# Optimization experiments

Hardware: AMD Instinct MI355X
Metric: run time of the kernel (lower is better)

## Reference

```python
import jax, jax.numpy as jnp
import numpy as np

M, B, T, C, H, HS = 2, 8, 1024, 512, 8, 64
EPS = 1e-5

NAMES = ['x','sa_kw1','sa_kb1','sa_kw2','sa_qw1','sa_qb1','sa_qw2','sa_vw1','sa_vb1','sa_vw2',
         'sa_pw1','sa_pb1','sa_pw2','sa_pb2','ff_w1','ff_b1','ff_w2','ff_b2',
         'ln1_g','ln1_b','ln2_g','ln2_b','lnc_g','lnc_b',
         'ca_qw','ca_kvw','ca_pw1','ca_pb1','ca_pw2','ca_pb2']


def setup_inputs() -> dict:
    key = jax.random.key(0)
    it = iter(jax.random.split(key, 40))
    def w(shape, s=0.02):
        return jax.random.normal(next(it), shape, jnp.float32) * s
    d = {}
    d['x'] = jax.random.normal(next(it), (M, B, T, C), jnp.float32)
    # self-attention heads: Linear(C,HS//2)+bias -> tanh -> Linear(HS//2,HS) no bias, stacked over (M,H)
    for nm in ('k', 'q', 'v'):
        d['sa_%sw1' % nm] = w((M, H, C, HS // 2))
        d['sa_%sb1' % nm] = jnp.zeros((M, H, HS // 2), jnp.float32)
        d['sa_%sw2' % nm] = w((M, H, HS // 2, HS))
    # MHA output proj: Linear(H*HS,C//2)->tanh->Linear(C//2,C)
    d['sa_pw1'] = w((M, H * HS, C // 2)); d['sa_pb1'] = jnp.zeros((M, C // 2), jnp.float32)
    d['sa_pw2'] = w((M, C // 2, C));      d['sa_pb2'] = jnp.zeros((M, C), jnp.float32)
    # feed-forward
    d['ff_w1'] = w((M, C, 4 * C)); d['ff_b1'] = jnp.zeros((M, 4 * C), jnp.float32)
    d['ff_w2'] = w((M, 4 * C, C)); d['ff_b2'] = jnp.zeros((M, C), jnp.float32)
    # layernorms
    for nm in ('ln1', 'ln2', 'lnc'):
        d[nm + '_g'] = jnp.ones((M, C), jnp.float32)
        d[nm + '_b'] = jnp.zeros((M, C), jnp.float32)
    # cross-attention: per head q proj (no bias), per-kv-modality kv proj (no bias, 2*HS)
    d['ca_qw'] = w((M, H, C, HS))
    d['ca_kvw'] = w((M, H, M - 1, C, 2 * HS))
    d['ca_pw1'] = w((M, H * HS, C // 2)); d['ca_pb1'] = jnp.zeros((M, C // 2), jnp.float32)
    d['ca_pw2'] = w((M, C // 2, C));      d['ca_pb2'] = jnp.zeros((M, C), jnp.float32)
    return d


def _ln(x, g, b):
    mu = x.mean(-1, keepdims=True)
    var = ((x - mu) ** 2).mean(-1, keepdims=True)
    return (x - mu) * jax.lax.rsqrt(var + EPS) * g + b


def _attend(q, k, v, mask):
    # q,k,v: (B,H,T,HS); causal masked softmax attention
    aff = jnp.einsum('bhtd,bhsd->bhts', q, k) * (HS ** -0.5)
    aff = jnp.where(mask, aff, -jnp.inf)
    return jnp.einsum('bhts,bhsd->bhtd', jax.nn.softmax(aff, axis=-1), v)


def _merge(o):
    # (B,H,T,HS) -> (B,T,H*HS), matching torch.cat over heads
    return o.transpose(0, 2, 1, 3).reshape(o.shape[0], o.shape[2], -1)


def _forward(p):
    mask = jnp.tril(jnp.ones((T, T), bool))
    x = p['x']
    attended = []
    for i in range(M):  # fixed small modality loop
        xi = x[i]
        h = _ln(xi, p['ln1_g'][i], p['ln1_b'][i])
        def hm(w1, b1, w2):
            # batched over heads: Linear->tanh->Linear
            z = jnp.tanh(jnp.einsum('btc,hce->bhte', h, w1) + b1[:, None, :])
            return jnp.einsum('bhte,hed->bhtd', z, w2)
        o = _attend(hm(p['sa_qw1'][i], p['sa_qb1'][i], p['sa_qw2'][i]),
                    hm(p['sa_kw1'][i], p['sa_kb1'][i], p['sa_kw2'][i]),
                    hm(p['sa_vw1'][i], p['sa_vb1'][i], p['sa_vw2'][i]), mask)
        o = jnp.tanh(_merge(o) @ p['sa_pw1'][i] + p['sa_pb1'][i]) @ p['sa_pw2'][i] + p['sa_pb2'][i]
        xi = xi + o
        h2 = _ln(xi, p['ln2_g'][i], p['ln2_b'][i])
        xi = xi + (jax.nn.relu(h2 @ p['ff_w1'][i] + p['ff_b1'][i]) @ p['ff_w2'][i] + p['ff_b2'][i])
        attended.append(xi)
    outs = []
    for i in range(M):
        xi = attended[i]
        hq = _ln(xi, p['lnc_g'][i], p['lnc_b'][i])
        q = jnp.einsum('btc,hcd->bhtd', hq, p['ca_qw'][i])
        acc = 0.0
        for jidx, j in enumerate([j for j in range(M) if j != i]):
            kv = jnp.einsum('btc,hcd->bhtd', attended[j], p['ca_kvw'][i][:, jidx])
            k, v = jnp.split(kv, 2, axis=-1)
            acc = acc + _attend(q, k, v, mask)
        o = jnp.tanh(_merge(acc) @ p['ca_pw1'][i] + p['ca_pb1'][i]) @ p['ca_pw2'][i] + p['ca_pb2'][i]
        outs.append(xi + o)
    return jnp.stack(outs)


def reference(x, sa_kw1, sa_kb1, sa_kw2, sa_qw1, sa_qb1, sa_qw2, sa_vw1, sa_vb1, sa_vw2,
              sa_pw1, sa_pb1, sa_pw2, sa_pb2, ff_w1, ff_b1, ff_w2, ff_b2,
              ln1_g, ln1_b, ln2_g, ln2_b, lnc_g, lnc_b,
              ca_qw, ca_kvw, ca_pw1, ca_pb1, ca_pw2, ca_pb2):
    args = (x, sa_kw1, sa_kb1, sa_kw2, sa_qw1, sa_qb1, sa_qw2, sa_vw1, sa_vb1, sa_vw2,
            sa_pw1, sa_pb1, sa_pw2, sa_pb2, ff_w1, ff_b1, ff_w2, ff_b2,
            ln1_g, ln1_b, ln2_g, ln2_b, lnc_g, lnc_b,
            ca_qw, ca_kvw, ca_pw1, ca_pb1, ca_pw2, ca_pb2)
    return _forward(dict(zip(NAMES, args)))
```

## Files before the change

### kernel.cpp

```cpp
#include <hip/hip_runtime.h>
#include <hip/hip_bf16.h>

#define DEVI __device__ __forceinline__

typedef __attribute__((ext_vector_type(8))) short short8v;
typedef __attribute__((ext_vector_type(4))) short short4v;
typedef __attribute__((ext_vector_type(4))) float float4v;
typedef __attribute__((ext_vector_type(16))) float f32x16;

#if defined(__has_builtin)
#if __has_builtin(__builtin_amdgcn_exp2f)
#define EXP2F(x) __builtin_amdgcn_exp2f(x)
#endif
#endif
#ifndef EXP2F
#define EXP2F(x) exp2f(x)
#endif

constexpr int Mm = 2, Bb = 8, Tt = 1024, Cc = 512, Hh = 8, HSs = 64;
constexpr int ROWS = Bb * Tt;
constexpr size_t BTC = (size_t)Bb * Tt * Cc;
constexpr size_t SLAB = (size_t)ROWS * 512;
constexpr size_t KOFF = (size_t)2 * ROWS * 768;
constexpr size_t VOFF = KOFF + 2 * SLAB;
constexpr float SCQ = 0.18033688011112042f;

DEVI short f2bf(float f) {
    __hip_bfloat16 h = __float2bfloat16(f);
    short s; __builtin_memcpy(&s, &h, 2); return s;
}

DEVI float4v mfma16(short8v a, short8v b, float4v c) {
    return __builtin_amdgcn_mfma_f32_16x16x32_bf16(a, b, c, 0, 0, 0);
}
DEVI f32x16 mfma32(short8v a, short8v b, f32x16 c) {
    return __builtin_amdgcn_mfma_f32_32x32x16_bf16(a, b, c, 0, 0, 0);
}

DEVI void gload_lds16(const short* g, short* l) {
    __builtin_amdgcn_global_load_lds(
        (const __attribute__((address_space(1))) void*)g,
        (__attribute__((address_space(3))) void*)l, 16, 0, 0);
}

struct TDesc {
    const float* src; short* dst;
    int K, N;
    long long moff, hoff;
    int base;
};
struct TPack { TDesc d[14]; };

__global__ __launch_bounds__(256) void transpose_all(TPack p) {
    __shared__ float t[32][33];
    int bid = blockIdx.x;
    int di = 0;
#pragma unroll
    for (int i = 1; i < 14; i++) if (bid >= p.d[i].base) di = i;
    TDesc d = p.d[di];
    int local = bid - d.base;
    int kb = d.K >> 5, nb = d.N >> 5;
    int bx = local % kb; int rest = local / kb;
    int by = rest % nb;  int z = rest / nb;
    int k0 = bx * 32, n0 = by * 32;
    size_t so = (size_t)z * d.K * d.N;
    short* dst = d.dst + (size_t)(z >> 3) * d.moff + (size_t)(z & 7) * d.hoff;
    int tx = threadIdx.x & 31, ty = threadIdx.x >> 5;
#pragma unroll
    for (int i = 0; i < 32; i += 8)
        t[ty + i][tx] = d.src[so + (size_t)(k0 + ty + i) * d.N + n0 + tx];
    __syncthreads();
#pragma unroll
    for (int i = 0; i < 32; i += 8)
        dst[(size_t)(n0 + ty + i) * d.K + k0 + tx] = f2bf(t[tx][ty + i]);
}

__global__ __launch_bounds__(256) void bias_cat3(const float* __restrict__ q,
                                                 const float* __restrict__ k,
                                                 const float* __restrict__ v,
                                                 float* __restrict__ o) {
    int m = blockIdx.x, t = threadIdx.x;
    o[m * 768 + t]       = q[m * 256 + t];
    o[m * 768 + 256 + t] = k[m * 256 + t];
    o[m * 768 + 512 + t] = v[m * 256 + t];
}

__global__ __launch_bounds__(256) void vtrans(const short* __restrict__ V,
                                              short* __restrict__ VT,
                                              int vrs, int hs, long long vzs) {
    __shared__ short t[32][33];
    int t0 = blockIdx.x * 32, d0 = blockIdx.y * 32;
    int z = blockIdx.z, mod = z >> 6, bh = z & 63, b = bh >> 3, h = bh & 7;
    const short* src = V + (long long)mod * vzs + (size_t)b * Tt * vrs + h * hs;
    short* dst = VT + (size_t)z * 65536;
    int tx = threadIdx.x, ty = threadIdx.y;
#pragma unroll
    for (int i = 0; i < 32; i += 8)
        t[ty + i][tx] = src[(size_t)(t0 + ty + i) * vrs + d0 + tx];
    __syncthreads();
#pragma unroll
    for (int i = 0; i < 32; i += 8)
        dst[(size_t)(d0 + ty + i) * Tt + t0 + tx] = t[tx][ty + i];
}

__global__ __launch_bounds__(256) void ln_kernel(const float* __restrict__ x,
                                                 const float* __restrict__ g,
                                                 const float* __restrict__ b,
                                                 short* __restrict__ out, size_t xzs) {
    int z = blockIdx.y;
    x += z * xzs; g += z * Cc; b += z * Cc; out += z * SLAB;
    int row = blockIdx.x * 4 + (threadIdx.x >> 6);
    int l = threadIdx.x & 63;
    const float* xr = x + (size_t)row * Cc;
    float4 a = *(const float4*)&xr[l * 4];
    float4 c = *(const float4*)&xr[256 + l * 4];
    float s = (a.x + a.y) + (a.z + a.w) + (c.x + c.y) + (c.z + c.w);
    float q = (a.x * a.x + a.y * a.y) + (a.z * a.z + a.w * a.w) +
              (c.x * c.x + c.y * c.y) + (c.z * c.z + c.w * c.w);
#pragma unroll
    for (int o = 1; o < 64; o <<= 1) { s += __shfl_xor(s, o, 64); q += __shfl_xor(q, o, 64); }
    float mu = s * (1.f / Cc);
    float var = q * (1.f / Cc) - mu * mu;
    float rs = rsqrtf(var + 1e-5f);
    float4 ga = *(const float4*)&g[l * 4],   gc = *(const float4*)&g[256 + l * 4];
    float4 ba = *(const float4*)&b[l * 4],   bc = *(const float4*)&b[256 + l * 4];
    short4v o1, o2;
    o1[0] = f2bf((a.x - mu) * rs * ga.x + ba.x);
    o1[1] = f2bf((a.y - mu) * rs * ga.y + ba.y);
    o1[2] = f2bf((a.z - mu) * rs * ga.z + ba.z);
    o1[3] = f2bf((a.w - mu) * rs * ga.w + ba.w);
    o2[0] = f2bf((c.x - mu) * rs * gc.x + bc.x);
    o2[1] = f2bf((c.y - mu) * rs * gc.y + bc.y);
    o2[2] = f2bf((c.z - mu) * rs * gc.z + bc.z);
    o2[3] = f2bf((c.w - mu) * rs * gc.w + bc.w);
    short* orow = out + (size_t)row * Cc;
    *(short4v*)&orow[l * 4]       = o1;
    *(short4v*)&orow[256 + l * 4] = o2;
}

template<int BM, int BN, int ACT, bool BIAS, bool RES, bool WF, bool WB>
__global__ __launch_bounds__(256, 2) void gemm2(
    const short* __restrict__ A, int lda, long long a_zs,
    const short* __restrict__ Wt, int ldw, long long w_zs,
    const float* __restrict__ bias, long long bias_zs,
    const float* __restrict__ res, long long res_zs,
    float* __restrict__ outF, long long outF_zs,
    short* __restrict__ outB, long long outB_zs,
    int ldc, int K, float oscale) {
    constexpr int BK = 64;
    __shared__ short As[BM][BK];
    __shared__ short Bs[BN][BK];
    long long z = blockIdx.z;
    A += z * a_zs; Wt += z * w_zs;
    if (BIAS) bias += z * bias_zs;
    if (RES)  res  += z * res_zs;
    if (WF)   outF += z * outF_zs;
    if (WB)   outB += z * outB_zs;
    int m0 = blockIdx.x * BM, n0 = blockIdx.y * BN;
    int tid = threadIdx.x, wv = tid >> 6, l = tid & 63, lr = l & 15, lg = l >> 4;
    constexpr int WM = BM / 2, WN = BN / 2;
    int wm = wv & 1, wn = wv >> 1;
    constexpr int AI = WM / 16, BJ = WN / 16;
    float4v acc[AI][BJ] = {};
    int lrow = l >> 3;
    int gcol = (l & 7) ^ lrow;
    constexpr int CHA = BM / 8, CHB = BN / 8;
    for (int k0 = 0; k0 < K; k0 += BK) {
        __syncthreads();
#pragma unroll
        for (int c = 0; c < CHA / 4; c++) {
            int ch = wv + c * 4;
            gload_lds16(&A[(size_t)(m0 + ch * 8 + lrow) * lda + k0 + gcol * 8],
                        &As[ch * 8][0]);
        }
#pragma unroll
        for (int c = 0; c < CHB / 4; c++) {
            int ch = wv + c * 4;
            gload_lds16(&Wt[(size_t)(n0 + ch * 8 + lrow) * ldw + k0 + gcol * 8],
                        &Bs[ch * 8][0]);
        }
        __syncthreads();
#pragma unroll
        for (int kk = 0; kk < 2; kk++) {
            int g = (kk * 4 + lg) ^ (lr & 7);
            short8v af[AI], bfv[BJ];
#pragma unroll
            for (int i = 0; i < AI; i++)
                af[i] = *(const short8v*)&As[wm * WM + i * 16 + lr][g * 8];
#pragma unroll
            for (int j = 0; j < BJ; j++)
                bfv[j] = *(const short8v*)&Bs[wn * WN + j * 16 + lr][g * 8];
#pragma unroll
            for (int i = 0; i < AI; i++)
#pragma unroll
                for (int j = 0; j < BJ; j++)
                    acc[i][j] = mfma16(af[i], bfv[j], acc[i][j]);
        }
    }
#pragma unroll
    for (int i = 0; i < AI; i++) {
#pragma unroll
        for (int j = 0; j < BJ; j++) {
            int col = n0 + wn * WN + j * 16 + lr;
            float bv = BIAS ? bias[col] : 0.f;
#pragma unroll
            for (int r = 0; r < 4; r++) {
                int row = m0 + wm * WM + i * 16 + lg * 4 + r;
                float v = acc[i][j][r] * oscale + bv;
                if (ACT == 1) v = tanhf(v);
                if (ACT == 2) v = fmaxf(v, 0.f);
                size_t idx = (size_t)row * ldc + col;
                if (RES) v += res[idx];
                if (WF) outF[idx] = v;
                if (WB) outB[idx] = f2bf(v);
            }
        }
    }
}

template<int ACT, bool BIAS, bool RES, bool WF, bool WB>
__global__ __launch_bounds__(256, 2) void gemm3(
    const short* __restrict__ A, int lda, long long a_zs,
    const short* __restrict__ Wt, int ldw, long long w_zs,
    const float* __restrict__ bias, long long bias_zs,
    const float* __restrict__ res, long long res_zs,
    float* __restrict__ outF, long long outF_zs,
    short* __restrict__ outB, long long outB_zs,
    int ldc, int K, float oscale) {
    constexpr int BM = 128, BN = 128, BK = 64;
    __shared__ short As[2][BM][BK];
    __shared__ short Bs[2][BN][BK];
    long long z = blockIdx.z;
    A += z * a_zs; Wt += z * w_zs;
    if (BIAS) bias += z * bias_zs;
    if (RES)  res  += z * res_zs;
    if (WF)   outF += z * outF_zs;
    if (WB)   outB += z * outB_zs;
    int m0 = blockIdx.x * BM, n0 = blockIdx.y * BN;
    int tid = threadIdx.x, wv = tid >> 6, l = tid & 63;
    int lq = l & 31, hi = l >> 5;
    int wm = wv & 1, wn = wv >> 1;
    f32x16 acc[2][2] = {};
    int lrow = l >> 3;
    int gcol = (l & 7) ^ lrow;

    auto STAGE = [&](int bi, int k0) {
#pragma unroll
        for (int c = 0; c < 4; c++) {
            int ch = wv + c * 4;
            gload_lds16(&A[(size_t)(m0 + ch * 8 + lrow) * lda + k0 + gcol * 8],
                        &As[bi][ch * 8][0]);
        }
#pragma unroll
        for (int c = 0; c < 4; c++) {
            int ch = wv + c * 4;
            gload_lds16(&Wt[(size_t)(n0 + ch * 8 + lrow) * ldw + k0 + gcol * 8],
                        &Bs[bi][ch * 8][0]);
        }
    };

    STAGE(0, 0);
    __syncthreads();
    int NT = K / BK;
    for (int t = 0; t < NT; t++) {
        int cur = t & 1;
        if (t + 1 < NT) STAGE(cur ^ 1, (t + 1) * BK);
        const short (*Ac)[BK] = As[cur];
        const short (*Bc)[BK] = Bs[cur];
#pragma unroll
        for (int ks = 0; ks < 4; ks++) {
            int g = (ks * 2 + hi) ^ (lq & 7);
            short8v af[2], bf[2];
#pragma unroll
            for (int i = 0; i < 2; i++)
                af[i] = *(const short8v*)&Ac[wm * 64 + i * 32 + lq][g * 8];
#pragma unroll
            for (int j = 0; j < 2; j++)
                bf[j] = *(const short8v*)&Bc[wn * 64 + j * 32 + lq][g * 8];
#pragma unroll
            for (int i = 0; i < 2; i++)
#pragma unroll
                for (int j = 0; j < 2; j++)
                    acc[i][j] = mfma32(af[i], bf[j], acc[i][j]);
        }
        __syncthreads();
    }
#pragma unroll
    for (int i = 0; i < 2; i++) {
#pragma unroll
        for (int j = 0; j < 2; j++) {
            int col = n0 + wn * 64 + j * 32 + lq;
            float bv = BIAS ? bias[col] : 0.f;
#pragma unroll
            for (int r = 0; r < 16; r++) {
                int row = m0 + wm * 64 + i * 32 + 4 * hi + (r & 3) + 8 * (r >> 2);
                float v = acc[i][j][r] * oscale + bv;
                if (ACT == 1) v = tanhf(v);
                if (ACT == 2) v = fmaxf(v, 0.f);
                size_t idx = (size_t)row * ldc + col;
                if (RES) v += res[idx];
                if (WF) outF[idx] = v;
                if (WB) outB[idx] = f2bf(v);
            }
        }
    }
}

__global__ __launch_bounds__(256) void proj2(const short* __restrict__ Z,
                                             const short* __restrict__ W2,
                                             short* __restrict__ Qo,
                                             short* __restrict__ Ko,
                                             short* __restrict__ VTo,
                                             float qscale) {
    __shared__ short As[64][40], Ws[64][40];
    __shared__ short Tv[64][72];
    int zz = blockIdx.y, t = zz >> 4, m = (zz >> 3) & 1, h = zz & 7;
    int m0 = blockIdx.x * 64;
    const short* Ap = Z + (size_t)m * ((size_t)ROWS * 768) + t * 256 + h * 32;
    const short* Wp = W2 + (size_t)zz * 2048;
    float sc = (t == 0) ? qscale : 1.0f;
    int tid = threadIdx.x, w = tid >> 6, l = tid & 63, lr = l & 15, lg = l >> 4;
    int r = tid >> 2, c = (tid & 3) * 8;
    *(short8v*)&As[r][c] = *(const short8v*)&Ap[(size_t)(m0 + r) * 768 + c];
    *(short8v*)&Ws[r][c] = *(const short8v*)&Wp[r * 32 + c];
    __syncthreads();
    short8v af = *(const short8v*)&As[w * 16 + lr][lg * 8];
    float4v acc[4] = {};
#pragma unroll
    for (int j = 0; j < 4; j++) {
        short8v bf = *(const short8v*)&Ws[j * 16 + lr][lg * 8];
        acc[j] = mfma16(af, bf, acc[j]);
    }
    if (t < 2) {
        short* Op = (t == 0 ? Qo : Ko) + (size_t)m * SLAB + h * 64;
#pragma unroll
        for (int j = 0; j < 4; j++)
#pragma unroll
            for (int rr = 0; rr < 4; rr++)
                Op[(size_t)(m0 + w * 16 + lg * 4 + rr) * 512 + j * 16 + lr] =
                    f2bf(acc[j][rr] * sc);
    } else {
#pragma unroll
        for (int j = 0; j < 4; j++)
#pragma unroll
            for (int rr = 0; rr < 4; rr++)
                Tv[j * 16 + lr][w * 16 + lg * 4 + rr] = f2bf(acc[j][rr]);
        __syncthreads();
        int b = m0 >> 10, trow0 = m0 & 1023;
        int z64 = m * 64 + b * 8 + h;
        short* dst = VTo + (size_t)z64 * 65536;
        int d = w * 16 + (l >> 2), toff = (l & 3) * 16;
        *(short8v*)&dst[(size_t)d * Tt + trow0 + toff]     = *(const short8v*)&Tv[d][toff];
        *(short8v*)&dst[(size_t)d * Tt + trow0 + toff + 8] = *(const short8v*)&Tv[d][toff + 8];
    }
}

__global__ __launch_bounds__(512, 4) void flash_attn4(
    const short* __restrict__ Q, const short* __restrict__ K,
    const short* __restrict__ VT, short* __restrict__ O,
    int krs, int khs, long long qzs, long long kzs, long long vtzs, long long ozs)
{
    __shared__ short Ks[2][64][64];
    __shared__ short Vs[2][64][64];
    int id = blockIdx.x;
    int bh = id & 63, mod = (id >> 6) & 1, p = (id >> 7) & 3;
    Q += (long long)mod * qzs; K += (long long)mod * kzs;
    VT += (long long)mod * vtzs; O += (long long)mod * ozs;
    int b = bh >> 3, h = bh & 7;
    int tid = threadIdx.x, w = tid >> 6, l = tid & 63;
    int lq = l & 31, hi = l >> 5;
    int strip = (w < 4) ? p : 7 - p;
    int qwb = strip * 128 + (w & 3) * 32;
    int qabs = qwb + lq;
    const short* Qp = Q + (size_t)b * Tt * Cc + h * HSs;
    const short* Kp = K + (size_t)b * Tt * krs + h * khs;
    const short* Vp = VT + (size_t)bh * HSs * Tt;
    short* Op = O + (size_t)b * Tt * Cc + h * HSs;

    short8v qf[4];
#pragma unroll
    for (int c = 0; c < 4; c++)
        qf[c] = *(const short8v*)&Qp[(size_t)qabs * Cc + (c * 2 + hi) * 8];

    f32x16 oacc[2] = {};
    float mrun = -1e30f, lrun = 0.f;
    int nk = 2 * (7 - p) + 2;
    short8v pk, pv;

    auto LOADT = [&](int kb) {
        int r = tid >> 3, cg = (tid & 7) ^ (r & 7);
        pk = *(const short8v*)&Kp[(size_t)(kb + r) * krs + cg * 8];
        pv = *(const short8v*)&Vp[(size_t)r * Tt + kb + cg * 8];
    };
    auto STORET = [&](int bi) {
        int r = tid >> 3, cp = tid & 7;
        *(short8v*)&Ks[bi][r][cp * 8] = pk;
        *(short8v*)&Vs[bi][r][cp * 8] = pv;
    };

    LOADT(0); STORET(0); __syncthreads();

    for (int t = 0; t < nk; t++) {
        int cur = t & 1, kb = t * 64;
        bool pre = (t + 1 < nk);
        if (pre) LOADT(kb + 64);
        if (kb <= qwb + 31) {
            bool full = (kb + 63 <= qwb);
            f32x16 st[2] = {};
            __builtin_amdgcn_s_setprio(1);
#pragma unroll
            for (int kh = 0; kh < 2; kh++) {
#pragma unroll
                for (int cc = 0; cc < 4; cc++) {
                    int r = kh * 32 + lq;
                    int cp = (cc * 2 + hi) ^ (r & 7);
                    short8v af = *(const short8v*)&Ks[cur][r][cp * 8];
                    st[kh] = mfma32(af, qf[cc], st[kh]);
                }
            }
            __builtin_amdgcn_s_setprio(0);
            float pr[32];
            if (full) {
#pragma unroll
                for (int kh = 0; kh < 2; kh++)
#pragma unroll
                    for (int r = 0; r < 16; r++) pr[kh * 16 + r] = st[kh][r];
            } else {
#pragma unroll
                for (int kh = 0; kh < 2; kh++)
#pragma unroll
                    for (int r = 0; r < 16; r++) {
                        int kabs = kb + kh * 32 + (r & 3) + 8 * (r >> 2) + 4 * hi;
                        pr[kh * 16 + r] = (kabs <= qabs) ? st[kh][r] : -3.0e38f;
                    }
            }
            float t16[16];
#pragma unroll
            for (int i = 0; i < 16; i++) t16[i] = fmaxf(pr[i], pr[i + 16]);
#pragma unroll
            for (int i = 0; i < 8; i++) t16[i] = fmaxf(t16[i], t16[i + 8]);
            float mx = fmaxf(fmaxf(fmaxf(t16[0], t16[4]), fmaxf(t16[1], t16[5])),
                             fmaxf(fmaxf(t16[2], t16[6]), fmaxf(t16[3], t16[7])));
            mx = fmaxf(mx, __shfl_xor(mx, 32));
            if (!__all(mx <= mrun + 11.5f)) {
                float mn = fmaxf(mrun, mx);
                float al = EXP2F(mrun - mn);
                mrun = mn;
                lrun *= al;
#pragma unroll
                for (int dh = 0; dh < 2; dh++)
#pragma unroll
                    for (int r = 0; r < 16; r++) oacc[dh][r] *= al;
            }
#pragma unroll
            for (int i = 0; i < 32; i++) pr[i] = EXP2F(pr[i] - mrun);
            float s16[16];
#pragma unroll
            for (int i = 0; i < 16; i++) s16[i] = pr[i] + pr[i + 16];
#pragma unroll
            for (int i = 0; i < 8; i++) s16[i] = s16[i] + s16[i + 8];
            float rsum = ((s16[0] + s16[4]) + (s16[1] + s16[5])) +
                         ((s16[2] + s16[6]) + (s16[3] + s16[7]));
            rsum += __shfl_xor(rsum, 32);
            lrun += rsum;
#pragma unroll
            for (int ks = 0; ks < 4; ks++) {
                unsigned x0, x1, y0, y1;
                asm("v_cvt_pk_bf16_f32 %0, %1, %2" : "=v"(x0) : "v"(pr[ks*8+0]), "v"(pr[ks*8+1]));
                asm("v_cvt_pk_bf16_f32 %0, %1, %2" : "=v"(x1) : "v"(pr[ks*8+2]), "v"(pr[ks*8+3]));
                asm("v_cvt_pk_bf16_f32 %0, %1, %2" : "=v"(y0) : "v"(pr[ks*8+4]), "v"(pr[ks*8+5]));
                asm("v_cvt_pk_bf16_f32 %0, %1, %2" : "=v"(y1) : "v"(pr[ks*8+6]), "v"(pr[ks*8+7]));
                asm volatile("v_permlane32_swap_b32 %0, %1" : "+v"(x0), "+v"(y0));
                asm volatile("v_permlane32_swap_b32 %0, %1" : "+v"(x1), "+v"(y1));
                union { unsigned u[4]; short8v s; } uu;
                uu.u[0] = x0; uu.u[1] = x1; uu.u[2] = y0; uu.u[3] = y1;
                __builtin_amdgcn_s_setprio(1);
#pragma unroll
                for (int dh = 0; dh < 2; dh++) {
                    int r = dh * 32 + lq;
                    int cp = (ks * 2 + hi) ^ (r & 7);
                    short8v vf = *(const short8v*)&Vs[cur][r][cp * 8];
                    oacc[dh] = mfma32(vf, uu.s, oacc[dh]);
                }
                __builtin_amdgcn_s_setprio(0);
            }
        }
        if (pre) STORET(cur ^ 1);
        __syncthreads();
    }
    float inv = 1.f / lrun;
#pragma unroll
    for (int dh = 0; dh < 2; dh++)
#pragma unroll
        for (int r = 0; r < 16; r += 2) {
            unsigned wds;
            float a0 = oacc[dh][r] * inv, a1 = oacc[dh][r + 1] * inv;
            asm("v_cvt_pk_bf16_f32 %0, %1, %2" : "=v"(wds) : "v"(a0), "v"(a1));
            int d = (r & 3) + 8 * (r >> 2) + 4 * hi + dh * 32;
            *(unsigned*)&Op[(size_t)qabs * Cc + d] = wds;
        }
}

extern "C" void kernel_launch(void* const* d_in, const int* in_sizes, int n_in,
                              void* d_out, int out_size, void* d_ws, size_t ws_size,
                              hipStream_t stream) {
    (void)in_sizes; (void)n_in; (void)out_size; (void)ws_size;
    const float* X     = (const float*)d_in[0];
    const float* saKW1 = (const float*)d_in[1];
    const float* saKB1 = (const float*)d_in[2];
    const float* saKW2 = (const float*)d_in[3];
    const float* saQW1 = (const float*)d_in[4];
    const float* saQB1 = (const float*)d_in[5];
    const float* saQW2 = (const float*)d_in[6];
    const float* saVW1 = (const float*)d_in[7];
    const float* saVB1 = (const float*)d_in[8];
    const float* saVW2 = (const float*)d_in[9];
    const float* saPW1 = (const float*)d_in[10];
    const float* saPB1 = (const float*)d_in[11];
    const float* saPW2 = (const float*)d_in[12];
    const float* saPB2 = (const float*)d_in[13];
    const float* ffW1  = (const float*)d_in[14];
    const float* ffB1  = (const float*)d_in[15];
    const float* ffW2  = (const float*)d_in[16];
    const float* ffB2  = (const float*)d_in[17];
    const float* ln1g  = (const float*)d_in[18];
    const float* ln1b  = (const float*)d_in[19];
    const float* ln2g  = (const float*)d_in[20];
    const float* ln2b  = (const float*)d_in[21];
    const float* lncg  = (const float*)d_in[22];
    const float* lncb  = (const float*)d_in[23];
    const float* caQW  = (const float*)d_in[24];
    const float* caKVW = (const float*)d_in[25];
    const float* caPW1 = (const float*)d_in[26];
    const float* caPB1 = (const float*)d_in[27];
    const float* caPW2 = (const float*)d_in[28];
    const float* caPB2 = (const float*)d_in[29];
    float* OUT = (float*)d_out;

    char* ws = (char*)d_ws;
    size_t cur = 0;
    auto alloc = [&](size_t bytes) -> char* {
        char* p = ws + cur; cur += (bytes + 255) & ~(size_t)255; return p;
    };

    short* WT = (short*)alloc((size_t)7700480 * 2);
    size_t wo = 0;
    auto wslot = [&](size_t e) -> short* { short* p = WT + wo; wo += e; return p; };
    short* w_qkv1 = wslot(786432);
    short* w_qkv2 = wslot(98304);
    short* w_pw1 = wslot(262144); short* w_pw2 = wslot(262144);
    short* w_ff1 = wslot(2097152); short* w_ff2 = wslot(2097152);
    short* w_caq = wslot(524288);  short* w_cakv = wslot(1048576);
    short* w_cp1 = wslot(262144);  short* w_cp2 = wslot(262144);
    float* bqkv = (float*)alloc(2 * 768 * 4);

    short* Hb  = (short*)alloc(2 * SLAB * 2);
    short* Qb  = (short*)alloc(2 * SLAB * 2);
    short* Obf = (short*)alloc(2 * SLAB * 2);
    short* Fb  = (short*)alloc((size_t)2 * ROWS * 2048 * 2);
    short* AB  = (short*)alloc(2 * SLAB * 2);
    short* VTb = Hb;
    short* P1b = Hb;
    short* Kb = Fb + KOFF;

    TPack tp;
    int base = 0, ti = 0;
    auto addT = [&](const float* s, short* d, int K, int N, int slices,
                    long long moff, long long hoff) {
        tp.d[ti++] = TDesc{s, d, K, N, moff, hoff, base};
        base += (K / 32) * (N / 32) * slices;
    };
    addT(saQW1, w_qkv1,          512, 32, 16, 393216, 16384);
    addT(saKW1, w_qkv1 + 131072, 512, 32, 16, 393216, 16384);
    addT(saVW1, w_qkv1 + 262144, 512, 32, 16, 393216, 16384);
    addT(saQW2, w_qkv2,          32, 64, 16, 16384, 2048);
    addT(saKW2, w_qkv2 + 32768,  32, 64, 16, 16384, 2048);
    addT(saVW2, w_qkv2 + 65536,  32, 64, 16, 16384, 2048);
    addT(saPW1, w_pw1, 512, 256, 2, 0, 131072);
    addT(saPW2, w_pw2, 256, 512, 2, 0, 131072);
    addT(ffW1,  w_ff1, 512, 2048, 2, 0, 1048576);
    addT(ffW2,  w_ff2, 2048, 512, 2, 0, 1048576);
    addT(caQW,  w_caq, 512, 64, 16, 262144, 32768);
    addT(caKVW, w_cakv, 512, 128, 16, 524288, 65536);
    addT(caPW1, w_cp1, 512, 256, 2, 0, 131072);
    addT(caPW2, w_cp2, 256, 512, 2, 0, 131072);
    transpose_all<<<dim3(base), 256, 0, stream>>>(tp);
    bias_cat3<<<2, 256, 0, stream>>>(saQB1, saKB1, saVB1, bqkv);

    dim3 tb32(32, 8, 1);

    ln_kernel<<<dim3(ROWS / 4, 2), 256, 0, stream>>>(X, ln1g, ln1b, Hb, BTC);
    gemm2<128, 128, 1, true, false, false, true><<<dim3(64, 6, 2), 256, 0, stream>>>(
        Hb, 512, SLAB, w_qkv1, 512, 393216, bqkv, 768,
        nullptr, 0, nullptr, 0, Fb, (long long)ROWS * 768, 768, 512, 1.0f);
    proj2<<<dim3(128, 48), 256, 0, stream>>>(Fb, w_qkv2, Qb, Kb, VTb, SCQ);
    flash_attn4<<<dim3(512), 512, 0, stream>>>(
        Qb, Kb, VTb, Obf, 512, 64, SLAB, SLAB, 4194304, SLAB);
    gemm2<64, 128, 1, true, false, false, true><<<dim3(128, 2, 2), 256, 0, stream>>>(
        Obf, 512, SLAB, w_pw1, 512, 131072, saPB1, 256,
        nullptr, 0, nullptr, 0, P1b, (long long)ROWS * 256, 256, 512, 1.0f);
    gemm2<64, 128, 0, true, true, true, false><<<dim3(128, 4, 2), 256, 0, stream>>>(
        P1b, 256, (long long)ROWS * 256, w_pw2, 256, 131072, saPB2, 512,
        X, BTC, OUT, BTC, nullptr, 0, 512, 256, 1.0f);
    ln_kernel<<<dim3(ROWS / 4, 2), 256, 0, stream>>>(OUT, ln2g, ln2b, Hb, BTC);
    gemm2<128, 128, 2, true, false, false, true><<<dim3(64, 16, 2), 256, 0, stream>>>(
        Hb, 512, SLAB, w_ff1, 512, 1048576, ffB1, 2048,
        nullptr, 0, nullptr, 0, Fb, (long long)ROWS * 2048, 2048, 512, 1.0f);
    gemm3<0, true, true, true, true><<<dim3(64, 4, 2), 256, 0, stream>>>(
        Fb, 2048, (long long)ROWS * 2048, w_ff2, 2048, 1048576, ffB2, 512,
        OUT, BTC, OUT, BTC, AB, SLAB, 512, 2048, 1.0f);

    ln_kernel<<<dim3(ROWS / 4, 2), 256, 0, stream>>>(OUT, lncg, lncb, Hb, BTC);
    gemm2<64, 128, 0, false, false, false, true><<<dim3(128, 4, 2), 256, 0, stream>>>(
        Hb, 512, SLAB, w_caq, 512, 262144, nullptr, 0,
        nullptr, 0, nullptr, 0, Qb, SLAB, 512, 512, SCQ);
    gemm2<128, 128, 0, false, false, false, true><<<dim3(64, 8, 2), 256, 0, stream>>>(
        AB + SLAB, 512, -(long long)SLAB, w_cakv, 512, 524288, nullptr, 0,
        nullptr, 0, nullptr, 0, Fb, (long long)ROWS * 1024, 1024, 512, 1.0f);
    vtrans<<<dim3(32, 2, 128), tb32, 0, stream>>>(Fb + 64, VTb, 1024, 128, (long long)ROWS * 1024);
    flash_attn4<<<dim3(512), 512, 0, stream>>>(
        Qb, Fb, VTb, Obf, 1024, 128, SLAB, (long long)ROWS * 1024, 4194304, SLAB);
    gemm2<64, 128, 1, true, false, false, true><<<dim3(128, 2, 2), 256, 0, stream>>>(
        Obf, 512, SLAB, w_cp1, 512, 131072, caPB1, 256,
        nullptr, 0, nullptr, 0, P1b, (long long)ROWS * 256, 256, 512, 1.0f);
    gemm2<64, 128, 0, true, true, true, false><<<dim3(128, 4, 2), 256, 0, stream>>>(
        P1b, 256, (long long)ROWS * 256, w_cp2, 256, 131072, caPB2, 512,
        OUT, BTC, OUT, BTC, nullptr, 0, 512, 256, 1.0f);
}
```

Baseline: 355.3 us.

## Fuse output-projection MLP pairs and fold V transpose into KV GEMM epilogue

Replaces each pair of output-projection GEMMs (Linear→tanh→Linear plus residual) with one kernel that keeps the 32x256 tanh intermediate in shared memory, avoiding a global round trip of the intermediate and one launch per projection. The cross-attention KV GEMM now writes K directly and transposes the V half through LDS in its epilogue, removing the separate vtrans kernel. The fused projection kernel reads A and weights straight from global memory without LDS staging, so the GEMM part may run at lower efficiency than the tiled gemm2 it replaces.

```diff
diff --git a/kernel.cpp b/kernel.cpp
--- a/kernel.cpp
+++ b/kernel.cpp
@@ -22,7 +22,6 @@
 constexpr size_t BTC = (size_t)Bb * Tt * Cc;
 constexpr size_t SLAB = (size_t)ROWS * 512;
 constexpr size_t KOFF = (size_t)2 * ROWS * 768;
-constexpr size_t VOFF = KOFF + 2 * SLAB;
 constexpr float SCQ = 0.18033688011112042f;
 
 DEVI short f2bf(float f) {
@@ -83,24 +82,6 @@
     o[m * 768 + t]       = q[m * 256 + t];
     o[m * 768 + 256 + t] = k[m * 256 + t];
     o[m * 768 + 512 + t] = v[m * 256 + t];
-}
-
-__global__ __launch_bounds__(256) void vtrans(const short* __restrict__ V,
-                                              short* __restrict__ VT,
-                                              int vrs, int hs, long long vzs) {
-    __shared__ short t[32][33];
-    int t0 = blockIdx.x * 32, d0 = blockIdx.y * 32;
-    int z = blockIdx.z, mod = z >> 6, bh = z & 63, b = bh >> 3, h = bh & 7;
-    const short* src = V + (long long)mod * vzs + (size_t)b * Tt * vrs + h * hs;
-    short* dst = VT + (size_t)z * 65536;
-    int tx = threadIdx.x, ty = threadIdx.y;
-#pragma unroll
-    for (int i = 0; i < 32; i += 8)
-        t[ty + i][tx] = src[(size_t)(t0 + ty + i) * vrs + d0 + tx];
-    __syncthreads();
-#pragma unroll
-    for (int i = 0; i < 32; i += 8)
-        dst[(size_t)(d0 + ty + i) * Tt + t0 + tx] = t[tx][ty + i];
 }
 
 __global__ __launch_bounds__(256) void ln_kernel(const float* __restrict__ x,
@@ -218,6 +199,88 @@
     }
 }
 
+__global__ __launch_bounds__(256, 2) void gemm_kv(
+    const short* __restrict__ A, long long a_zs,
+    const short* __restrict__ Wt, long long w_zs,
+    short* __restrict__ outB, long long outB_zs,
+    short* __restrict__ VTo, int K) {
+    constexpr int BK = 64;
+    __shared__ short As[128][BK];
+    __shared__ short Bs[128][BK];
+    __shared__ short Tv[64][136];
+    long long z = blockIdx.z;
+    A += z * a_zs; Wt += z * w_zs; outB += z * outB_zs;
+    int m0 = blockIdx.x * 128, n0 = blockIdx.y * 128;
+    int tid = threadIdx.x, wv = tid >> 6, l = tid & 63, lr = l & 15, lg = l >> 4;
+    int wm = wv & 1, wn = wv >> 1;
+    float4v acc[4][4] = {};
+    int lrow = l >> 3;
+    int gcol = (l & 7) ^ lrow;
+    for (int k0 = 0; k0 < K; k0 += BK) {
+        __syncthreads();
+#pragma unroll
+        for (int c = 0; c < 4; c++) {
+            int ch = wv + c * 4;
+            gload_lds16(&A[(size_t)(m0 + ch * 8 + lrow) * 512 + k0 + gcol * 8],
+                        &As[ch * 8][0]);
+        }
+#pragma unroll
+        for (int c = 0; c < 4; c++) {
+            int ch = wv + c * 4;
+            gload_lds16(&Wt[(size_t)(n0 + ch * 8 + lrow) * 512 + k0 + gcol * 8],
+                        &Bs[ch * 8][0]);
+        }
+        __syncthreads();
+#pragma unroll
+        for (int kk = 0; kk < 2; kk++) {
+            int g = (kk * 4 + lg) ^ (lr & 7);
+            short8v af[4], bfv[4];
+#pragma unroll
+            for (int i = 0; i < 4; i++)
+                af[i] = *(const short8v*)&As[wm * 64 + i * 16 + lr][g * 8];
+#pragma unroll
+            for (int j = 0; j < 4; j++)
+                bfv[j] = *(const short8v*)&Bs[wn * 64 + j * 16 + lr][g * 8];
+#pragma unroll
+            for (int i = 0; i < 4; i++)
+#pragma unroll
+                for (int j = 0; j < 4; j++)
+                    acc[i][j] = mfma16(af[i], bfv[j], acc[i][j]);
+        }
+    }
+    if (wn == 0) {
+#pragma unroll
+        for (int i = 0; i < 4; i++)
+#pragma unroll
+            for (int j = 0; j < 4; j++) {
+                int col = n0 + j * 16 + lr;
+#pragma unroll
+                for (int r = 0; r < 4; r++) {
+                    int row = m0 + wm * 64 + i * 16 + lg * 4 + r;
+                    outB[(size_t)row * 1024 + col] = f2bf(acc[i][j][r]);
+                }
+            }
+    } else {
+#pragma unroll
+        for (int i = 0; i < 4; i++)
+#pragma unroll
+            for (int j = 0; j < 4; j++) {
+                int d = j * 16 + lr;
+#pragma unroll
+                for (int r = 0; r < 4; r++)
+                    Tv[d][wm * 64 + i * 16 + lg * 4 + r] = f2bf(acc[i][j][r]);
+            }
+    }
+    __syncthreads();
+    int b = m0 >> 10, trow0 = m0 & 1023, h = n0 >> 7;
+    short* dst = VTo + (size_t)(blockIdx.z * 64 + b * 8 + h) * 65536;
+    int d = tid >> 2, c0 = (tid & 3) * 32;
+#pragma unroll
+    for (int q = 0; q < 4; q++)
+        *(short8v*)&dst[(size_t)d * Tt + trow0 + c0 + q * 8] =
+            *(const short8v*)&Tv[d][c0 + q * 8];
+}
+
 template<int ACT, bool BIAS, bool RES, bool WF, bool WB>
 __global__ __launch_bounds__(256, 2) void gemm3(
     const short* __restrict__ A, int lda, long long a_zs,
@@ -304,6 +367,77 @@
             }
         }
     }
+}
+
+__global__ __launch_bounds__(256, 2) void proj_fused(
+    const short* __restrict__ A,
+    const short* __restrict__ W1t,
+    const float* __restrict__ B1,
+    const short* __restrict__ W2t,
+    const float* __restrict__ B2,
+    const float* __restrict__ res,
+    float* __restrict__ outF) {
+    __shared__ short P1s[32][264];
+    long long z = blockIdx.y;
+    A += z * SLAB; W1t += z * 131072; B1 += z * 256;
+    W2t += z * 131072; B2 += z * 512;
+    res += z * BTC; outF += z * BTC;
+    int m0 = blockIdx.x * 32;
+    int tid = threadIdx.x, wv = tid >> 6, l = tid & 63, lr = l & 15, lg = l >> 4;
+    float4v acc[2][4] = {};
+    for (int k0 = 0; k0 < 512; k0 += 32) {
+        short8v af[2], bf[4];
+#pragma unroll
+        for (int i = 0; i < 2; i++)
+            af[i] = *(const short8v*)&A[(size_t)(m0 + i * 16 + lr) * 512 + k0 + lg * 8];
+#pragma unroll
+        for (int j = 0; j < 4; j++)
+            bf[j] = *(const short8v*)&W1t[(size_t)(wv * 64 + j * 16 + lr) * 512 + k0 + lg * 8];
+#pragma unroll
+        for (int i = 0; i < 2; i++)
+#pragma unroll
+            for (int j = 0; j < 4; j++)
+                acc[i][j] = mfma16(af[i], bf[j], acc[i][j]);
+    }
+#pragma unroll
+    for (int i = 0; i < 2; i++)
+#pragma unroll
+        for (int j = 0; j < 4; j++) {
+            int col = wv * 64 + j * 16 + lr;
+            float bv = B1[col];
+#pragma unroll
+            for (int r = 0; r < 4; r++)
+                P1s[i * 16 + lg * 4 + r][col] = f2bf(tanhf(acc[i][j][r] + bv));
+        }
+    __syncthreads();
+    float4v acc2[2][8] = {};
+    for (int k0 = 0; k0 < 256; k0 += 32) {
+        short8v af[2], bf[8];
+#pragma unroll
+        for (int i = 0; i < 2; i++)
+            af[i] = *(const short8v*)&P1s[i * 16 + lr][k0 + lg * 8];
+#pragma unroll
+        for (int j = 0; j < 8; j++)
+            bf[j] = *(const short8v*)&W2t[(size_t)(wv * 128 + j * 16 + lr) * 256 + k0 + lg * 8];
+#pragma unroll
+        for (int i = 0; i < 2; i++)
+#pragma unroll
+            for (int j = 0; j < 8; j++)
+                acc2[i][j] = mfma16(af[i], bf[j], acc2[i][j]);
+    }
+#pragma unroll
+    for (int i = 0; i < 2; i++)
+#pragma unroll
+        for (int j = 0; j < 8; j++) {
+            int col = wv * 128 + j * 16 + lr;
+            float bv = B2[col];
+#pragma unroll
+            for (int r = 0; r < 4; r++) {
+                int row = m0 + i * 16 + lg * 4 + r;
+                size_t idx = (size_t)row * 512 + col;
+                outF[idx] = acc2[i][j][r] + bv + res[idx];
+            }
+        }
 }
 
 __global__ __launch_bounds__(256) void proj2(const short* __restrict__ Z,
@@ -560,7 +694,6 @@
     short* Fb  = (short*)alloc((size_t)2 * ROWS * 2048 * 2);
     short* AB  = (short*)alloc(2 * SLAB * 2);
     short* VTb = Hb;
-    short* P1b = Hb;
     short* Kb = Fb + KOFF;
 
     TPack tp;
@@ -587,8 +720,6 @@
     transpose_all<<<dim3(base), 256, 0, stream>>>(tp);
     bias_cat3<<<2, 256, 0, stream>>>(saQB1, saKB1, saVB1, bqkv);
 
-    dim3 tb32(32, 8, 1);
-
     ln_kernel<<<dim3(ROWS / 4, 2), 256, 0, stream>>>(X, ln1g, ln1b, Hb, BTC);
     gemm2<128, 128, 1, true, false, false, true><<<dim3(64, 6, 2), 256, 0, stream>>>(
         Hb, 512, SLAB, w_qkv1, 512, 393216, bqkv, 768,
@@ -596,12 +727,8 @@
     proj2<<<dim3(128, 48), 256, 0, stream>>>(Fb, w_qkv2, Qb, Kb, VTb, SCQ);
     flash_attn4<<<dim3(512), 512, 0, stream>>>(
         Qb, Kb, VTb, Obf, 512, 64, SLAB, SLAB, 4194304, SLAB);
-    gemm2<64, 128, 1, true, false, false, true><<<dim3(128, 2, 2), 256, 0, stream>>>(
-        Obf, 512, SLAB, w_pw1, 512, 131072, saPB1, 256,
-        nullptr, 0, nullptr, 0, P1b, (long long)ROWS * 256, 256, 512, 1.0f);
-    gemm2<64, 128, 0, true, true, true, false><<<dim3(128, 4, 2), 256, 0, stream>>>(
-        P1b, 256, (long long)ROWS * 256, w_pw2, 256, 131072, saPB2, 512,
-        X, BTC, OUT, BTC, nullptr, 0, 512, 256, 1.0f);
+    proj_fused<<<dim3(256, 2), 256, 0, stream>>>(
+        Obf, w_pw1, saPB1, w_pw2, saPB2, X, OUT);
     ln_kernel<<<dim3(ROWS / 4, 2), 256, 0, stream>>>(OUT, ln2g, ln2b, Hb, BTC);
     gemm2<128, 128, 2, true, false, false, true><<<dim3(64, 16, 2), 256, 0, stream>>>(
         Hb, 512, SLAB, w_ff1, 512, 1048576, ffB1, 2048,
@@ -614,16 +741,11 @@
     gemm2<64, 128, 0, false, false, false, true><<<dim3(128, 4, 2), 256, 0, stream>>>(
         Hb, 512, SLAB, w_caq, 512, 262144, nullptr, 0,
         nullptr, 0, nullptr, 0, Qb, SLAB, 512, 512, SCQ);
-    gemm2<128, 128, 0, false, false, false, true><<<dim3(64, 8, 2), 256, 0, stream>>>(
-        AB + SLAB, 512, -(long long)SLAB, w_cakv, 512, 524288, nullptr, 0,
-        nullptr, 0, nullptr, 0, Fb, (long long)ROWS * 1024, 1024, 512, 1.0f);
-    vtrans<<<dim3(32, 2, 128), tb32, 0, stream>>>(Fb + 64, VTb, 1024, 128, (long long)ROWS * 1024);
+    gemm_kv<<<dim3(64, 8, 2), 256, 0, stream>>>(
+        AB + SLAB, -(long long)SLAB, w_cakv, 524288,
+        Fb, (long long)ROWS * 1024, VTb, 512);
     flash_attn4<<<dim3(512), 512, 0, stream>>>(
         Qb, Fb, VTb, Obf, 1024, 128, SLAB, (long long)ROWS * 1024, 4194304, SLAB);
-    gemm2<64, 128, 1, true, false, false, true><<<dim3(128, 2, 2), 256, 0, stream>>>(
-        Obf, 512, SLAB, w_cp1, 512, 131072, caPB1, 256,
-        nullptr, 0, nullptr, 0, P1b, (long long)ROWS * 256, 256, 512, 1.0f);
-    gemm2<64, 128, 0, true, true, true, false><<<dim3(128, 4, 2), 256, 0, stream>>>(
-        P1b, 256, (long long)ROWS * 256, w_cp2, 256, 131072, caPB2, 512,
-        OUT, BTC, OUT, BTC, nullptr, 0, 512, 256, 1.0f);
-}
+    proj_fused<<<dim3(256, 2), 256, 0, stream>>>(
+        Obf, w_cp1, caPB1, w_cp2, caPB2, OUT, OUT);
+}
```

After: 390.4 us. 9.9% more time.
